# Optimization experiments

Measured on AMD Instinct MI355X. Metric: run time of the kernel, lower is better.

The kernel has to match this reference:

```python
import jax, jax.numpy as jnp
import numpy as np

N = 1_048_576   # flattened tokens
C = 128         # classes
IGNORE = 0
GAMMA = 1.0     # FocalLoss bug: alpha default (1) becomes self.gamma
BETA = 1.0      # ClassficationAndMDCA: self.beta = alpha = 1.0


def setup_inputs() -> dict:
    key = jax.random.key(0)
    k1, k2 = jax.random.split(key)
    inputs = jax.random.normal(k1, (N, C), dtype=jnp.float32)
    targets = jax.random.randint(k2, (N,), 0, C, dtype=jnp.int64)
    return {"inputs": inputs, "targets": targets}


def reference(inputs, targets):
    # ignore_index filtering expressed as masked reductions (jit-friendly)
    mask = (targets != IGNORE)
    maskf = mask.astype(inputs.dtype)               # [N]
    nvalid = jnp.sum(maskf)

    # Focal loss: -(1-pt)^gamma * log pt, mean over valid tokens
    logp = jax.nn.log_softmax(inputs, axis=1)       # [N, C]
    logpt = jnp.take_along_axis(logp, targets[:, None], axis=1)[:, 0]  # [N]
    pt = jnp.exp(logpt)
    focal = -((1.0 - pt) ** GAMMA) * logpt
    loss_cls = jnp.sum(focal * maskf) / nvalid

    # MDCA: per-class |mean confidence - mean label frequency|, mean over classes
    probs = jnp.exp(logp)                           # softmax, reuse log_softmax
    avg_conf = jnp.sum(probs * maskf[:, None], axis=0) / nvalid        # [C]
    avg_count = jnp.zeros((C,), inputs.dtype).at[targets].add(maskf) / nvalid  # [C]
    loss_cal = jnp.mean(jnp.abs(avg_conf - avg_count))

    return loss_cls + BETA * loss_cal
```

## Files before the change

### kernel.cpp

```cpp
#include <hip/hip_runtime.h>

#define NC 128
#define BLOCK 256
#define GRID 2048

typedef float f32x4 __attribute__((ext_vector_type(4)));

__global__ void cmdca_init(float* __restrict__ acc) {
    if (threadIdx.x < 260) acc[threadIdx.x] = 0.0f;
}

template <int CTRL>
__device__ __forceinline__ float dpp_add(float v) {
    int s = __builtin_amdgcn_update_dpp(0, __float_as_int(v), CTRL, 0xF, 0xF, true);
    return v + __int_as_float(s);
}
__device__ __forceinline__ float rowsum16(float v) {
    v = dpp_add<0x121>(v);
    v = dpp_add<0x122>(v);
    v = dpp_add<0x124>(v);
    v = dpp_add<0x128>(v);
    return v;
}

__global__ __launch_bounds__(BLOCK) void cmdca_main(const float* __restrict__ in,
                                                    const int* __restrict__ tgt,
                                                    float* __restrict__ acc,
                                                    int nrows) {
    const int lane = threadIdx.x & 63;
    const int l15  = lane & 15;
    const int sub  = lane >> 4;
    const int wave = blockIdx.x * (BLOCK >> 6) + (threadIdx.x >> 6);
    const int nwaves = GRID * (BLOCK >> 6);
    const int qtot = (nrows + 3) >> 2;

    __shared__ float sconf[NC];
    __shared__ float scnt[NC];
    __shared__ float sfn[2];
    for (int i = threadIdx.x; i < NC; i += BLOCK) { sconf[i] = 0.f; scnt[i] = 0.f; }
    if (threadIdx.x < 2) sfn[threadIdx.x] = 0.f;
    __syncthreads();

    float conf[8] = {0.f, 0.f, 0.f, 0.f, 0.f, 0.f, 0.f, 0.f};
    float focal = 0.f, nval = 0.f;

    struct Quad { f32x4 a, b; int t; };
    auto load = [&](int q, Quad& d) {
        int r = min(q * 4 + sub, nrows - 1);
        const float* p = in + (size_t)r * NC + l15 * 8;
        d.a = *reinterpret_cast<const f32x4*>(p);
        d.b = *reinterpret_cast<const f32x4*>(p + 4);
        d.t = tgt[r];
    };

    auto compute = [&](const Quad& d, int q) {
        const int t = d.t;
        const float x0 = d.a.x, x1 = d.a.y, x2 = d.a.z, x3 = d.a.w;
        const float x4 = d.b.x, x5 = d.b.y, x6 = d.b.z, x7 = d.b.w;
        const int te = t & 7;
        float s01 = (te & 1) ? x1 : x0;
        float s23 = (te & 1) ? x3 : x2;
        float s45 = (te & 1) ? x5 : x4;
        float s67 = (te & 1) ? x7 : x6;
        float s03 = (te & 2) ? s23 : s01;
        float s47 = (te & 2) ? s67 : s45;
        float xsel = (te & 4) ? s47 : s03;
        float e0 = __expf(x0), e1 = __expf(x1), e2 = __expf(x2), e3 = __expf(x3);
        float e4 = __expf(x4), e5 = __expf(x5), e6 = __expf(x6), e7 = __expf(x7);
        float s8 = ((e0 + e1) + (e2 + e3)) + ((e4 + e5) + (e6 + e7));
        float s = rowsum16(s8);
        float invs = __builtin_amdgcn_rcpf(s);
        float logZ = __logf(s);
        int srcl = (lane & 48) | (t >> 3);
        float xt = __int_as_float(
            __builtin_amdgcn_ds_bpermute(srcl << 2, __float_as_int(xsel)));
        float logpt = xt - logZ;
        float pt = __expf(logpt);
        float valid = (t != 0 && (q * 4 + sub) < nrows) ? 1.0f : 0.0f;
        float vs = valid * invs;
        conf[0] += vs * e0; conf[1] += vs * e1; conf[2] += vs * e2; conf[3] += vs * e3;
        conf[4] += vs * e4; conf[5] += vs * e5; conf[6] += vs * e6; conf[7] += vs * e7;
        if (l15 == 0) {
            nval  += valid;
            focal += valid * (pt - 1.0f) * logpt;
            if (valid != 0.0f) atomicAdd(&scnt[t], 1.0f);
        }
    };

    int q = wave;
    if (q < qtot) {
        Quad A; load(q, A);
        for (; q + nwaves < qtot; q += nwaves) {
            Quad B; load(q + nwaves, B);
            compute(A, q);
            A = B;
        }
        compute(A, q);
    }

    __syncthreads();
    const int cb = 8 * l15;
    atomicAdd(&sconf[cb + 0], conf[0]);
    atomicAdd(&sconf[cb + 1], conf[1]);
    atomicAdd(&sconf[cb + 2], conf[2]);
    atomicAdd(&sconf[cb + 3], conf[3]);
    atomicAdd(&sconf[cb + 4], conf[4]);
    atomicAdd(&sconf[cb + 5], conf[5]);
    atomicAdd(&sconf[cb + 6], conf[6]);
    atomicAdd(&sconf[cb + 7], conf[7]);
    if (l15 == 0) {
        atomicAdd(&sfn[0], focal);
        atomicAdd(&sfn[1], nval);
    }
    __syncthreads();
    if (threadIdx.x < NC) {
        atomicAdd(&acc[threadIdx.x],      sconf[threadIdx.x]);
        atomicAdd(&acc[NC + threadIdx.x], scnt[threadIdx.x]);
    }
    if (threadIdx.x == 0) {
        atomicAdd(&acc[2 * NC],     sfn[0]);
        atomicAdd(&acc[2 * NC + 1], sfn[1]);
    }
}

__global__ void cmdca_fin(const float* __restrict__ acc, float* __restrict__ out) {
    int c = threadIdx.x;
    float nvalid = acc[2 * NC + 1];
    float diff = fabsf(acc[c] - acc[NC + c]) / nvalid;
    #pragma unroll
    for (int o = 32; o; o >>= 1) diff += __shfl_xor(diff, o);
    __shared__ float sh[2];
    if ((threadIdx.x & 63) == 0) sh[threadIdx.x >> 6] = diff;
    __syncthreads();
    if (threadIdx.x == 0) {
        float loss_cal = (sh[0] + sh[1]) / (float)NC;
        float loss_cls = acc[2 * NC] / nvalid;
        out[0] = loss_cls + loss_cal;
    }
}

extern "C" void kernel_launch(void* const* d_in, const int* in_sizes, int n_in,
                              void* d_out, int out_size, void* d_ws, size_t ws_size,
                              hipStream_t stream) {
    const float* in  = (const float*)d_in[0];
    const int*   tgt = (const int*)d_in[1];
    float* out = (float*)d_out;
    float* acc = (float*)d_ws;
    int nrows = in_sizes[0] / NC;

    hipLaunchKernelGGL(cmdca_init, dim3(1), dim3(512), 0, stream, acc);
    hipLaunchKernelGGL(cmdca_main, dim3(GRID), dim3(BLOCK), 0, stream, in, tgt, acc, nrows);
    hipLaunchKernelGGL(cmdca_fin,  dim3(1), dim3(NC), 0, stream, acc, out);
}
```

Baseline: 132.8 us.

## Fuse finalize into main kernel via last-block counter and use contiguous per-block chunks

Drops the separate finalize kernel: each block bumps a counter in the workspace after a threadfence, and the last block reads the accumulators atomically and writes the scalar loss. Rows are now assigned to each block as a contiguous chunk of quads instead of a grid-stride spread, which should improve DRAM locality. It also adds a launch_bounds occupancy hint and recomputes the exps rather than keeping them live, to save registers. The intent is to remove one kernel launch and reduce register pressure, at the cost of recomputing eight exps per row and relying on the init kernel to zero the counter slot at index 258.

```diff
diff --git a/kernel.cpp b/kernel.cpp
--- a/kernel.cpp
+++ b/kernel.cpp
@@ -23,20 +23,24 @@
     return v;
 }
 
-__global__ __launch_bounds__(BLOCK) void cmdca_main(const float* __restrict__ in,
-                                                    const int* __restrict__ tgt,
-                                                    float* __restrict__ acc,
-                                                    int nrows) {
+__global__ __launch_bounds__(BLOCK, 4) void cmdca_main(const float* __restrict__ in,
+                                                       const int* __restrict__ tgt,
+                                                       float* __restrict__ acc,
+                                                       float* __restrict__ out,
+                                                       int nrows) {
     const int lane = threadIdx.x & 63;
     const int l15  = lane & 15;
     const int sub  = lane >> 4;
-    const int wave = blockIdx.x * (BLOCK >> 6) + (threadIdx.x >> 6);
-    const int nwaves = GRID * (BLOCK >> 6);
+    const int wid  = threadIdx.x >> 6;
     const int qtot = (nrows + 3) >> 2;
+    const int chunk = (qtot + GRID - 1) / GRID;
+    const int qbeg  = blockIdx.x * chunk;
+    const int qend  = min(qbeg + chunk, qtot);
 
     __shared__ float sconf[NC];
     __shared__ float scnt[NC];
     __shared__ float sfn[2];
+    __shared__ int slast;
     for (int i = threadIdx.x; i < NC; i += BLOCK) { sconf[i] = 0.f; scnt[i] = 0.f; }
     if (threadIdx.x < 2) sfn[threadIdx.x] = 0.f;
     __syncthreads();
@@ -44,30 +48,25 @@
     float conf[8] = {0.f, 0.f, 0.f, 0.f, 0.f, 0.f, 0.f, 0.f};
     float focal = 0.f, nval = 0.f;
 
-    struct Quad { f32x4 a, b; int t; };
-    auto load = [&](int q, Quad& d) {
+    auto load = [&](int q, f32x4& a, f32x4& b, int& t) {
         int r = min(q * 4 + sub, nrows - 1);
         const float* p = in + (size_t)r * NC + l15 * 8;
-        d.a = *reinterpret_cast<const f32x4*>(p);
-        d.b = *reinterpret_cast<const f32x4*>(p + 4);
-        d.t = tgt[r];
+        a = *reinterpret_cast<const f32x4*>(p);
+        b = *reinterpret_cast<const f32x4*>(p + 4);
+        t = tgt[r];
     };
 
-    auto compute = [&](const Quad& d, int q) {
-        const int t = d.t;
-        const float x0 = d.a.x, x1 = d.a.y, x2 = d.a.z, x3 = d.a.w;
-        const float x4 = d.b.x, x5 = d.b.y, x6 = d.b.z, x7 = d.b.w;
+    auto compute = [&](f32x4 xa, f32x4 xb, int t, int q) {
         const int te = t & 7;
-        float s01 = (te & 1) ? x1 : x0;
-        float s23 = (te & 1) ? x3 : x2;
-        float s45 = (te & 1) ? x5 : x4;
-        float s67 = (te & 1) ? x7 : x6;
+        float s01 = (te & 1) ? xa.y : xa.x;
+        float s23 = (te & 1) ? xa.w : xa.z;
+        float s45 = (te & 1) ? xb.y : xb.x;
+        float s67 = (te & 1) ? xb.w : xb.z;
         float s03 = (te & 2) ? s23 : s01;
         float s47 = (te & 2) ? s67 : s45;
         float xsel = (te & 4) ? s47 : s03;
-        float e0 = __expf(x0), e1 = __expf(x1), e2 = __expf(x2), e3 = __expf(x3);
-        float e4 = __expf(x4), e5 = __expf(x5), e6 = __expf(x6), e7 = __expf(x7);
-        float s8 = ((e0 + e1) + (e2 + e3)) + ((e4 + e5) + (e6 + e7));
+        float s8 = ((__expf(xa.x) + __expf(xa.y)) + (__expf(xa.z) + __expf(xa.w)))
+                 + ((__expf(xb.x) + __expf(xb.y)) + (__expf(xb.z) + __expf(xb.w)));
         float s = rowsum16(s8);
         float invs = __builtin_amdgcn_rcpf(s);
         float logZ = __logf(s);
@@ -78,8 +77,14 @@
         float pt = __expf(logpt);
         float valid = (t != 0 && (q * 4 + sub) < nrows) ? 1.0f : 0.0f;
         float vs = valid * invs;
-        conf[0] += vs * e0; conf[1] += vs * e1; conf[2] += vs * e2; conf[3] += vs * e3;
-        conf[4] += vs * e4; conf[5] += vs * e5; conf[6] += vs * e6; conf[7] += vs * e7;
+        conf[0] += vs * __expf(xa.x);
+        conf[1] += vs * __expf(xa.y);
+        conf[2] += vs * __expf(xa.z);
+        conf[3] += vs * __expf(xa.w);
+        conf[4] += vs * __expf(xb.x);
+        conf[5] += vs * __expf(xb.y);
+        conf[6] += vs * __expf(xb.z);
+        conf[7] += vs * __expf(xb.w);
         if (l15 == 0) {
             nval  += valid;
             focal += valid * (pt - 1.0f) * logpt;
@@ -87,15 +92,17 @@
         }
     };
 
-    int q = wave;
-    if (q < qtot) {
-        Quad A; load(q, A);
-        for (; q + nwaves < qtot; q += nwaves) {
-            Quad B; load(q + nwaves, B);
-            compute(A, q);
-            A = B;
+    int q = qbeg + wid;
+    if (q < qend) {
+        f32x4 xa, xb; int t;
+        load(q, xa, xb, t);
+        for (; q + 4 < qend; q += 4) {
+            f32x4 ya, yb; int u;
+            load(q + 4, ya, yb, u);
+            compute(xa, xb, t, q);
+            xa = ya; xb = yb; t = u;
         }
-        compute(A, q);
+        compute(xa, xb, t, q);
     }
 
     __syncthreads();
@@ -121,21 +128,28 @@
         atomicAdd(&acc[2 * NC],     sfn[0]);
         atomicAdd(&acc[2 * NC + 1], sfn[1]);
     }
-}
 
-__global__ void cmdca_fin(const float* __restrict__ acc, float* __restrict__ out) {
-    int c = threadIdx.x;
-    float nvalid = acc[2 * NC + 1];
-    float diff = fabsf(acc[c] - acc[NC + c]) / nvalid;
-    #pragma unroll
-    for (int o = 32; o; o >>= 1) diff += __shfl_xor(diff, o);
-    __shared__ float sh[2];
-    if ((threadIdx.x & 63) == 0) sh[threadIdx.x >> 6] = diff;
+    __threadfence();
     __syncthreads();
     if (threadIdx.x == 0) {
-        float loss_cal = (sh[0] + sh[1]) / (float)NC;
-        float loss_cls = acc[2 * NC] / nvalid;
-        out[0] = loss_cls + loss_cal;
+        unsigned old = atomicAdd(reinterpret_cast<unsigned*>(&acc[258]), 1u);
+        slast = (old == (unsigned)(gridDim.x - 1));
+    }
+    __syncthreads();
+    if (slast) {
+        if (threadIdx.x < NC) {
+            float c = atomicAdd(&acc[threadIdx.x], 0.f);
+            float k = atomicAdd(&acc[NC + threadIdx.x], 0.f);
+            sconf[threadIdx.x] = fabsf(c - k);
+        }
+        __syncthreads();
+        if (threadIdx.x == 0) {
+            float fo = atomicAdd(&acc[2 * NC], 0.f);
+            float nv = atomicAdd(&acc[2 * NC + 1], 0.f);
+            float sum = 0.f;
+            for (int i = 0; i < NC; ++i) sum += sconf[i];
+            out[0] = fo / nv + sum / (nv * (float)NC);
+        }
     }
 }
 
@@ -149,6 +163,6 @@
     int nrows = in_sizes[0] / NC;
 
     hipLaunchKernelGGL(cmdca_init, dim3(1), dim3(512), 0, stream, acc);
-    hipLaunchKernelGGL(cmdca_main, dim3(GRID), dim3(BLOCK), 0, stream, in, tgt, acc, nrows);
-    hipLaunchKernelGGL(cmdca_fin,  dim3(1), dim3(NC), 0, stream, acc, out);
+    hipLaunchKernelGGL(cmdca_main, dim3(GRID), dim3(BLOCK), 0, stream,
+                       in, tgt, acc, out, nrows);
 }
```

Measured after the change: 408.2 us. 3.07x slower.

## Stage input rows through LDS with a 4-deep global_load_lds pipeline

Applied to the files above, without the earlier changes.

Replaces the register double-buffered loads with direct global-to-LDS asynchronous loads (global_load_lds) into a per-wave 4-slot ring buffer, using explicit vmcnt waits to keep three quads in flight. The grid is halved so each wave handles more quads. The goal is deeper memory-level parallelism and better hiding of HBM latency on this bandwidth-bound reduction. In exchange it adds LDS traffic and about 40KB of LDS per block, which lowers occupancy. It also drops the tail-row handling, so nrows must be a multiple of 4. There is no wave-level barrier between an LDS slot being read and the same slot being refilled, which relies on in-order execution.

```diff
diff --git a/kernel.cpp b/kernel.cpp
--- a/kernel.cpp
+++ b/kernel.cpp
@@ -2,7 +2,10 @@
 
 #define NC 128
 #define BLOCK 256
-#define GRID 2048
+#define GRID 1024
+#define DEPTH 4
+#define QBYTES 2048
+#define WPB (BLOCK / 64)
 
 typedef float f32x4 __attribute__((ext_vector_type(4)));
 
@@ -30,13 +33,20 @@
     const int lane = threadIdx.x & 63;
     const int l15  = lane & 15;
     const int sub  = lane >> 4;
-    const int wave = blockIdx.x * (BLOCK >> 6) + (threadIdx.x >> 6);
-    const int nwaves = GRID * (BLOCK >> 6);
-    const int qtot = (nrows + 3) >> 2;
+    const int wid  = threadIdx.x >> 6;
+    const int wave = blockIdx.x * WPB + wid;
+    const int nwaves = GRID * WPB;
+    const int qtot = nrows >> 2;
 
+    __shared__ char  stage[WPB * DEPTH * QBYTES];
+    __shared__ int   tstage[WPB * DEPTH * 64];
     __shared__ float sconf[NC];
     __shared__ float scnt[NC];
     __shared__ float sfn[2];
+
+    char* wstage = stage  + wid * DEPTH * QBYTES;
+    int*  wts    = tstage + wid * DEPTH * 64;
+
     for (int i = threadIdx.x; i < NC; i += BLOCK) { sconf[i] = 0.f; scnt[i] = 0.f; }
     if (threadIdx.x < 2) sfn[threadIdx.x] = 0.f;
     __syncthreads();
@@ -44,29 +54,40 @@
     float conf[8] = {0.f, 0.f, 0.f, 0.f, 0.f, 0.f, 0.f, 0.f};
     float focal = 0.f, nval = 0.f;
 
-    struct Quad { f32x4 a, b; int t; };
-    auto load = [&](int q, Quad& d) {
-        int r = min(q * 4 + sub, nrows - 1);
-        const float* p = in + (size_t)r * NC + l15 * 8;
-        d.a = *reinterpret_cast<const f32x4*>(p);
-        d.b = *reinterpret_cast<const f32x4*>(p + 4);
-        d.t = tgt[r];
+    const int n = (qtot > wave) ? (qtot - 1 - wave) / nwaves + 1 : 0;
+
+    auto stg = [&](int j, int slot) {
+        size_t q = (size_t)wave + (size_t)j * nwaves;
+        const char* g = (const char*)in + q * QBYTES + lane * 16;
+        __builtin_amdgcn_global_load_lds(
+            (const __attribute__((address_space(1))) void*)g,
+            (__attribute__((address_space(3))) void*)(wstage + slot * QBYTES),
+            16, 0, 0);
+        __builtin_amdgcn_global_load_lds(
+            (const __attribute__((address_space(1))) void*)(g + 1024),
+            (__attribute__((address_space(3))) void*)(wstage + slot * QBYTES + 1024),
+            16, 0, 0);
+        __builtin_amdgcn_global_load_lds(
+            (const __attribute__((address_space(1))) void*)(tgt + 4 * q + (lane & 3)),
+            (__attribute__((address_space(3))) void*)(wts + slot * 64),
+            4, 0, 0);
     };
 
-    auto compute = [&](const Quad& d, int q) {
-        const int t = d.t;
-        const float x0 = d.a.x, x1 = d.a.y, x2 = d.a.z, x3 = d.a.w;
-        const float x4 = d.b.x, x5 = d.b.y, x6 = d.b.z, x7 = d.b.w;
+    auto cmp = [&](int slot) {
+        const char* b = wstage + slot * QBYTES + sub * 512 + l15 * 32;
+        f32x4 xa = *(const f32x4*)b;
+        f32x4 xb = *(const f32x4*)(b + 16);
+        int t = wts[slot * 64 + sub];
         const int te = t & 7;
-        float s01 = (te & 1) ? x1 : x0;
-        float s23 = (te & 1) ? x3 : x2;
-        float s45 = (te & 1) ? x5 : x4;
-        float s67 = (te & 1) ? x7 : x6;
+        float s01 = (te & 1) ? xa.y : xa.x;
+        float s23 = (te & 1) ? xa.w : xa.z;
+        float s45 = (te & 1) ? xb.y : xb.x;
+        float s67 = (te & 1) ? xb.w : xb.z;
         float s03 = (te & 2) ? s23 : s01;
         float s47 = (te & 2) ? s67 : s45;
         float xsel = (te & 4) ? s47 : s03;
-        float e0 = __expf(x0), e1 = __expf(x1), e2 = __expf(x2), e3 = __expf(x3);
-        float e4 = __expf(x4), e5 = __expf(x5), e6 = __expf(x6), e7 = __expf(x7);
+        float e0 = __expf(xa.x), e1 = __expf(xa.y), e2 = __expf(xa.z), e3 = __expf(xa.w);
+        float e4 = __expf(xb.x), e5 = __expf(xb.y), e6 = __expf(xb.z), e7 = __expf(xb.w);
         float s8 = ((e0 + e1) + (e2 + e3)) + ((e4 + e5) + (e6 + e7));
         float s = rowsum16(s8);
         float invs = __builtin_amdgcn_rcpf(s);
@@ -76,7 +97,7 @@
             __builtin_amdgcn_ds_bpermute(srcl << 2, __float_as_int(xsel)));
         float logpt = xt - logZ;
         float pt = __expf(logpt);
-        float valid = (t != 0 && (q * 4 + sub) < nrows) ? 1.0f : 0.0f;
+        float valid = (t != 0) ? 1.0f : 0.0f;
         float vs = valid * invs;
         conf[0] += vs * e0; conf[1] += vs * e1; conf[2] += vs * e2; conf[3] += vs * e3;
         conf[4] += vs * e4; conf[5] += vs * e5; conf[6] += vs * e6; conf[7] += vs * e7;
@@ -87,15 +108,19 @@
         }
     };
 
-    int q = wave;
-    if (q < qtot) {
-        Quad A; load(q, A);
-        for (; q + nwaves < qtot; q += nwaves) {
-            Quad B; load(q + nwaves, B);
-            compute(A, q);
-            A = B;
-        }
-        compute(A, q);
+    for (int jp = 0; jp < n && jp < DEPTH - 1; ++jp) stg(jp, jp);
+    int j = 0;
+    for (; j + (DEPTH - 1) < n; ++j) {
+        stg(j + DEPTH - 1, (j + DEPTH - 1) & (DEPTH - 1));
+        asm volatile("s_waitcnt vmcnt(9)" ::: "memory");
+        cmp(j & (DEPTH - 1));
+    }
+    for (; j < n; ++j) {
+        int after = n - 1 - j;
+        if (after >= 2)      { asm volatile("s_waitcnt vmcnt(6)" ::: "memory"); }
+        else if (after == 1) { asm volatile("s_waitcnt vmcnt(3)" ::: "memory"); }
+        else                 { asm volatile("s_waitcnt vmcnt(0)" ::: "memory"); }
+        cmp(j & (DEPTH - 1));
     }
 
     __syncthreads();
```

New measurement: 117.7 us (median of 2 runs). 1.13x faster.
